# Kernel tuning notes

Hardware: AMD Instinct MI355X
Metric: run time of the kernel (lower is better)

The kernel has to match this reference:

```python
import jax, jax.numpy as jnp
import numpy as np

# Dimensions
N, C_IN, C_OUT, T, V = 64, 64, 64, 256, 25   # batch, channels, frames, joints
K, G = 3, 8                                   # num_subset, groups


def batch_norm(x, gamma, beta, eps=1e-5):
    # BatchNorm2d in training mode: biased batch stats over (N, T, V) per channel.
    mean = jnp.mean(x, axis=(0, 2, 3), keepdims=True)
    var = jnp.var(x, axis=(0, 2, 3), keepdims=True)
    g = gamma.reshape(1, -1, 1, 1)
    b = beta.reshape(1, -1, 1, 1)
    return g * (x - mean) * jax.lax.rsqrt(var + eps) + b


def setup_inputs() -> dict:
    key = jax.random.key(0)
    k0, k1, k2 = jax.random.split(key, 3)
    x0 = jax.random.normal(k0, (N, C_IN, T, V), dtype=jnp.float32)
    # decoupled adjacency parameter [num_subset, groups, V, V] (non-negative, adjacency-like)
    decoupled_A = jax.random.uniform(k1, (K, G, V, V), dtype=jnp.float32)
    scale = float(np.sqrt(0.5 / (C_OUT * K)))
    linear_weight = jax.random.normal(k2, (C_IN, C_OUT * K), dtype=jnp.float32) * scale
    linear_bias = jnp.full((1, C_OUT * K, 1, 1), 1e-6, dtype=jnp.float32)
    bn0_gamma = jnp.ones((C_OUT * K,), dtype=jnp.float32)
    bn0_beta = jnp.zeros((C_OUT * K,), dtype=jnp.float32)
    bn_gamma = jnp.ones((C_OUT,), dtype=jnp.float32)
    bn_beta = jnp.zeros((C_OUT,), dtype=jnp.float32)
    return {
        "x0": x0,
        "decoupled_A": decoupled_A,
        "linear_weight": linear_weight,
        "linear_bias": linear_bias,
        "bn0_gamma": bn0_gamma,
        "bn0_beta": bn0_beta,
        "bn_gamma": bn_gamma,
        "bn_beta": bn_beta,
    }


def reference(x0, decoupled_A, linear_weight, linear_bias,
              bn0_gamma, bn0_beta, bn_gamma, bn_beta):
    # Expand grouped adjacency to per-output-channel: [K, C_OUT, V, V]
    learn_adj = jnp.tile(decoupled_A, (1, C_OUT // G, 1, 1))
    # Degree normalization: A @ diag(1/(colsum+1e-3)) == divide columns by column sums.
    deg = jnp.sum(learn_adj, axis=2, keepdims=True)          # [K, C_OUT, 1, V]
    normed_adj = learn_adj / (deg + 0.001)                    # [K, C_OUT, V, V]

    # Pointwise channel mix: [N, C_IN, T, V] -> [N, K*C_OUT, T, V]
    x = jnp.einsum('nctw,cd->ndtw', x0, linear_weight) + linear_bias
    x = batch_norm(x, bn0_gamma, bn0_beta)

    n, kc, t, v = x.shape
    x = x.reshape(n, K, kc // K, t, v)                        # [N, K, C_OUT, T, V]
    # Per-channel graph propagation summed over subsets.
    x = jnp.einsum('nkctv,kcvw->nctw', x, normed_adj)         # [N, C_OUT, T, V]
    x = batch_norm(x, bn_gamma, bn_beta)

    x = x + x0  # identity residual (in_channels == out_channels)
    return jax.nn.relu(x)
```

## Files before the change

kernel.cpp:

```cpp
#include <hip/hip_runtime.h>
#include <hip/hip_bf16.h>

#define N_    64
#define CIN   64
#define COUT  64
#define T_    256
#define V_    25
#define K_    3
#define G_    8
#define D_    192
#define TV    6400
#define P_    409600.0f

typedef __attribute__((ext_vector_type(8))) short bf16x8;
typedef __attribute__((ext_vector_type(4))) float f32x4;

__device__ __forceinline__ float bf2f(unsigned short u) {
    unsigned int x = ((unsigned int)u) << 16;
    return __uint_as_float(x);
}
__device__ __forceinline__ unsigned short f2bf(float f) {
    unsigned int x = __float_as_uint(f);
    unsigned int lsb = (x >> 16) & 1u;
    x += 0x7fffu + lsb;
    return (unsigned short)(x >> 16);
}

__global__ __launch_bounds__(256, 4) void k1_mfma(const float* __restrict__ x0,
                                                  const float* __restrict__ W,
                                                  const float* __restrict__ bias,
                                                  unsigned short* __restrict__ z) {
    int p0  = blockIdx.x * 256;
    int n   = p0 / TV;
    int tvb = p0 % TV;
    int wv  = threadIdx.x >> 6;
    int l   = threadIdx.x & 63;
    int l15 = l & 15;
    int kg  = l >> 4;
    int wbase = tvb + wv * 64;
    const float* xn = x0 + (size_t)n * CIN * TV;

    bf16x8 afr[4][2];
#pragma unroll
    for (int m = 0; m < 4; ++m)
#pragma unroll
        for (int kk = 0; kk < 2; ++kk)
#pragma unroll
            for (int j = 0; j < 8; ++j) {
                int c = kk * 32 + kg * 8 + j;
                afr[m][kk][j] = (short)f2bf(xn[(size_t)c * TV + wbase + m * 16 + l15]);
            }

    unsigned short* zn = z + (size_t)n * D_ * TV;
#pragma unroll 1
    for (int dt = 0; dt < 12; ++dt) {
        int dcol = dt * 16 + l15;
        bf16x8 bfr[2];
#pragma unroll
        for (int kk = 0; kk < 2; ++kk)
#pragma unroll
            for (int j = 0; j < 8; ++j) {
                int c = kk * 32 + kg * 8 + j;
                bfr[kk][j] = (short)f2bf(W[c * D_ + dcol]);
            }
        float bv = bias[dcol];
        f32x4 acc[4];
#pragma unroll
        for (int m = 0; m < 4; ++m) {
            acc[m][0] = bv; acc[m][1] = bv; acc[m][2] = bv; acc[m][3] = bv;
        }
#pragma unroll
        for (int m = 0; m < 4; ++m) {
            acc[m] = __builtin_amdgcn_mfma_f32_16x16x32_bf16(afr[m][0], bfr[0], acc[m], 0, 0, 0);
            acc[m] = __builtin_amdgcn_mfma_f32_16x16x32_bf16(afr[m][1], bfr[1], acc[m], 0, 0, 0);
        }
        unsigned short* zp = zn + (size_t)dcol * TV;
#pragma unroll
        for (int m = 0; m < 4; ++m) {
            int tv0 = wbase + m * 16 + kg * 4;
            uint2 pk;
            pk.x = (unsigned int)f2bf(acc[m][0]) | ((unsigned int)f2bf(acc[m][1]) << 16);
            pk.y = (unsigned int)f2bf(acc[m][2]) | ((unsigned int)f2bf(acc[m][3]) << 16);
            *(uint2*)(zp + tv0) = pk;
        }
    }
}

__global__ __launch_bounds__(256) void k1b_stats(const unsigned short* __restrict__ z,
                                                 float* __restrict__ sum0,
                                                 float* __restrict__ sumsq0) {
    int d    = blockIdx.x;
    int slab = blockIdx.y;
    float s = 0.f, sq = 0.f;
    for (int n = slab * 8; n < slab * 8 + 8; ++n) {
        const ushort4* zp = (const ushort4*)(z + ((size_t)n * D_ + d) * TV);
        for (int i = threadIdx.x; i < TV / 4; i += 256) {
            ushort4 u = zp[i];
            float a0 = bf2f(u.x), a1 = bf2f(u.y), a2 = bf2f(u.z), a3 = bf2f(u.w);
            s  += (a0 + a1) + (a2 + a3);
            sq += (a0 * a0 + a1 * a1) + (a2 * a2 + a3 * a3);
        }
    }
    __shared__ float rs[256], rq[256];
    rs[threadIdx.x] = s; rq[threadIdx.x] = sq;
    __syncthreads();
    for (int off = 128; off > 0; off >>= 1) {
        if (threadIdx.x < off) {
            rs[threadIdx.x] += rs[threadIdx.x + off];
            rq[threadIdx.x] += rq[threadIdx.x + off];
        }
        __syncthreads();
    }
    if (threadIdx.x == 0) {
        atomicAdd(&sum0[d], rs[0]);
        atomicAdd(&sumsq0[d], rq[0]);
    }
}

__global__ __launch_bounds__(256, 1) void k2_prep(const float* __restrict__ A,
                                                  const float* __restrict__ g0,
                                                  const float* __restrict__ b0,
                                                  const float* __restrict__ sum0,
                                                  const float* __restrict__ sumsq0,
                                                  float* a, float* b,
                                                  float* nadj, float* bconst) {
    int tid = threadIdx.x;
    if (tid < D_) {
        float m   = sum0[tid] / P_;
        float var = sumsq0[tid] / P_ - m * m;
        float sc  = g0[tid] * rsqrtf(var + 1e-5f);
        a[tid] = sc;
        b[tid] = b0[tid] - sc * m;
    }
    for (int idx = tid; idx < K_ * G_ * V_; idx += 256) {
        int w  = idx % V_;
        int kg = idx / V_;
        const float* Ap = A + kg * V_ * V_;
        float cs = 0.f;
        for (int v = 0; v < V_; ++v) cs += Ap[v * V_ + w];
        float inv = 1.f / (cs + 1e-3f);
        for (int v = 0; v < V_; ++v) nadj[kg * V_ * V_ + v * V_ + w] = Ap[v * V_ + w] * inv;
    }
    __syncthreads();
    for (int idx = tid; idx < COUT * V_; idx += 256) {
        int c = idx / V_, w = idx % V_, g = c & 7;
        float s = 0.f;
        for (int k = 0; k < K_; ++k) {
            float bk = b[k * COUT + c];
            const float* np_ = nadj + (k * G_ + g) * V_ * V_;
            float cs = 0.f;
            for (int v = 0; v < V_; ++v) cs += np_[v * V_ + w];
            s += bk * cs;
        }
        bconst[idx] = s;
    }
}

__global__ __launch_bounds__(256, 2) void k3_adj(const unsigned short* __restrict__ z,
                                                 const float* __restrict__ a,
                                                 const float* __restrict__ nadj,
                                                 const float* __restrict__ bconst,
                                                 unsigned short* __restrict__ x2,
                                                 float* __restrict__ sum2,
                                                 float* __restrict__ sumsq2) {
    __shared__ float s_nadj[K_][625];
    __shared__ __align__(16) unsigned short zs[4][TV];
    int tid = threadIdx.x;
    int g   = blockIdx.x & 7;
    int pq  = blockIdx.x >> 3;
    int wv  = tid >> 6;
    int l   = tid & 63;
    int p   = pq * 4 + wv;
    int n   = p >> 3;
    int c   = (p & 7) * 8 + g;
    for (int idx = tid; idx < K_ * 625; idx += 256) {
        int k = idx / 625, r = idx % 625;
        s_nadj[k][r] = nadj[(k * 8 + g) * 625 + r];
    }
    __syncthreads();

    float acc[4][25];
#pragma unroll
    for (int w = 0; w < 25; ++w) {
        float bc = bconst[c * 25 + w];
#pragma unroll
        for (int j = 0; j < 4; ++j) acc[j][w] = bc;
    }

    uint4* zs4 = (uint4*)&zs[wv][0];
#pragma unroll 1
    for (int k = 0; k < K_; ++k) {
        int d = k * 64 + c;
        const uint4* row4 = (const uint4*)(z + ((size_t)n * D_ + d) * TV);
        for (int e = l; e < 800; e += 64) zs4[e] = row4[e];
        float ad = a[d];
#pragma unroll 1
        for (int v = 0; v < 25; ++v) {
            float za0 = ad * bf2f(zs[wv][(l      ) * 25 + v]);
            float za1 = ad * bf2f(zs[wv][(l +  64) * 25 + v]);
            float za2 = ad * bf2f(zs[wv][(l + 128) * 25 + v]);
            float za3 = ad * bf2f(zs[wv][(l + 192) * 25 + v]);
            const float* nr = &s_nadj[k][v * 25];
#pragma unroll
            for (int w = 0; w < 25; ++w) {
                float nv = nr[w];
                acc[0][w] = fmaf(za0, nv, acc[0][w]);
                acc[1][w] = fmaf(za1, nv, acc[1][w]);
                acc[2][w] = fmaf(za2, nv, acc[2][w]);
                acc[3][w] = fmaf(za3, nv, acc[3][w]);
            }
        }
    }

    unsigned short* xp = x2 + ((size_t)n * COUT + c) * TV;
    float s = 0.f, sq = 0.f;
#pragma unroll
    for (int j = 0; j < 4; ++j) {
        int t = l + 64 * j;
#pragma unroll
        for (int w = 0; w < 25; ++w) {
            float val = acc[j][w];
            s += val; sq += val * val;
            xp[t * 25 + w] = f2bf(val);
        }
    }
#pragma unroll
    for (int off = 32; off > 0; off >>= 1) {
        s  += __shfl_down(s,  off, 64);
        sq += __shfl_down(sq, off, 64);
    }
    if (l == 0) {
        atomicAdd(&sum2[c], s);
        atomicAdd(&sumsq2[c], sq);
    }
}

__global__ __launch_bounds__(256) void k4_final(const unsigned short* __restrict__ x2,
                                                const float* __restrict__ x0,
                                                const float* __restrict__ g2,
                                                const float* __restrict__ b2,
                                                const float* __restrict__ sum2,
                                                const float* __restrict__ sumsq2,
                                                float* __restrict__ out) {
    const int total4 = N_ * COUT * TV / 4;
    for (int i = blockIdx.x * 256 + threadIdx.x; i < total4; i += gridDim.x * 256) {
        int c = ((i * 4) / TV) & 63;
        float m   = sum2[c] * (1.f / P_);
        float var = sumsq2[c] * (1.f / P_) - m * m;
        float sc  = g2[c] * rsqrtf(var + 1e-5f);
        float sh  = b2[c] - sc * m;
        ushort4 u = ((const ushort4*)x2)[i];
        float4  x = ((const float4*)x0)[i];
        float4 o;
        o.x = fmaxf(sc * bf2f(u.x) + sh + x.x, 0.f);
        o.y = fmaxf(sc * bf2f(u.y) + sh + x.y, 0.f);
        o.z = fmaxf(sc * bf2f(u.z) + sh + x.z, 0.f);
        o.w = fmaxf(sc * bf2f(u.w) + sh + x.w, 0.f);
        ((float4*)out)[i] = o;
    }
}

extern "C" void kernel_launch(void* const* d_in, const int* in_sizes, int n_in,
                              void* d_out, int out_size, void* d_ws, size_t ws_size,
                              hipStream_t stream) {
    const float* x0   = (const float*)d_in[0];
    const float* A    = (const float*)d_in[1];
    const float* W    = (const float*)d_in[2];
    const float* bias = (const float*)d_in[3];
    const float* g0   = (const float*)d_in[4];
    const float* b0   = (const float*)d_in[5];
    const float* g2   = (const float*)d_in[6];
    const float* b2   = (const float*)d_in[7];

    char* ws = (char*)d_ws;
    unsigned short* z  = (unsigned short*)ws;
    unsigned short* x2 = (unsigned short*)(ws + 157286400ull);
    float* fregion = (float*)(ws + 209715200ull);
    float* sum0   = fregion;
    float* sumsq0 = fregion + 192;
    float* sum2   = fregion + 384;
    float* sumsq2 = fregion + 448;
    float* a      = fregion + 512;
    float* b      = a + 192;
    float* nadj   = b + 192;
    float* bconst = nadj + 15000;

    hipMemsetAsync(fregion, 0, 512 * sizeof(float), stream);
    k1_mfma<<<1600, 256, 0, stream>>>(x0, W, bias, z);
    k1b_stats<<<dim3(D_, 8), 256, 0, stream>>>(z, sum0, sumsq0);
    k2_prep<<<1, 256, 0, stream>>>(A, g0, b0, sum0, sumsq0, a, b, nadj, bconst);
    k3_adj<<<1024, 256, 0, stream>>>(z, a, nadj, bconst, x2, sum2, sumsq2);
    k4_final<<<2048, 256, 0, stream>>>(x2, x0, g2, b2, sum2, sumsq2,
                                       (float*)d_out);
}
```

Baseline: 429.3 us.

## Fuse BN0 statistics into GEMM epilogue and stage z stores through LDS

Per-channel sum and sum-of-squares for the first batch norm are now computed from the fp32 MFMA accumulators inside the GEMM kernel. Per-block partials are written to a scratch buffer, and a small kernel reduces them deterministically. This removes the separate pass that re-read the whole bf16 intermediate z to get the statistics. Output tiles are also transposed through shared memory so the global stores are wider and contiguous. Statistics now come from unrounded fp32 values rather than the bf16-rounded z, which slightly changes numerics.

```diff
diff --git a/kernel.cpp b/kernel.cpp
--- a/kernel.cpp
+++ b/kernel.cpp
@@ -11,6 +11,7 @@
 #define D_    192
 #define TV    6400
 #define P_    409600.0f
+#define NBLK1 1600
 
 typedef __attribute__((ext_vector_type(8))) short bf16x8;
 typedef __attribute__((ext_vector_type(4))) float f32x4;
@@ -29,7 +30,10 @@
 __global__ __launch_bounds__(256, 4) void k1_mfma(const float* __restrict__ x0,
                                                   const float* __restrict__ W,
                                                   const float* __restrict__ bias,
-                                                  unsigned short* __restrict__ z) {
+                                                  unsigned short* __restrict__ z,
+                                                  float* __restrict__ part) {
+    __shared__ unsigned short zb[4][16 * 68];
+    __shared__ float ps[4][12][16], pq[4][12][16];
     int p0  = blockIdx.x * 256;
     int n   = p0 / TV;
     int tvb = p0 % TV;
@@ -52,6 +56,7 @@
             }
 
     unsigned short* zn = z + (size_t)n * D_ * TV;
+    unsigned short* zw = &zb[wv][0];
 #pragma unroll 1
     for (int dt = 0; dt < 12; ++dt) {
         int dcol = dt * 16 + l15;
@@ -74,46 +79,55 @@
             acc[m] = __builtin_amdgcn_mfma_f32_16x16x32_bf16(afr[m][0], bfr[0], acc[m], 0, 0, 0);
             acc[m] = __builtin_amdgcn_mfma_f32_16x16x32_bf16(afr[m][1], bfr[1], acc[m], 0, 0, 0);
         }
-        unsigned short* zp = zn + (size_t)dcol * TV;
+        float s = 0.f, sq = 0.f;
+#pragma unroll
+        for (int m = 0; m < 4; ++m)
+#pragma unroll
+            for (int r = 0; r < 4; ++r) {
+                float v = acc[m][r];
+                s += v; sq += v * v;
+            }
+        s  += __shfl_xor(s, 16, 64);  s  += __shfl_xor(s, 32, 64);
+        sq += __shfl_xor(sq, 16, 64); sq += __shfl_xor(sq, 32, 64);
+        if (kg == 0) { ps[wv][dt][l15] = s; pq[wv][dt][l15] = sq; }
 #pragma unroll
         for (int m = 0; m < 4; ++m) {
-            int tv0 = wbase + m * 16 + kg * 4;
             uint2 pk;
             pk.x = (unsigned int)f2bf(acc[m][0]) | ((unsigned int)f2bf(acc[m][1]) << 16);
             pk.y = (unsigned int)f2bf(acc[m][2]) | ((unsigned int)f2bf(acc[m][3]) << 16);
-            *(uint2*)(zp + tv0) = pk;
-        }
-    }
-}
-
-__global__ __launch_bounds__(256) void k1b_stats(const unsigned short* __restrict__ z,
+            *(uint2*)(&zw[l15 * 68 + m * 16 + kg * 4]) = pk;
+        }
+#pragma unroll
+        for (int i = 0; i < 4; ++i) {
+            int dR  = i * 4 + kg;
+            int tvo = l15 * 4;
+            uint2 v = *(const uint2*)(&zw[dR * 68 + tvo]);
+            *(uint2*)(zn + (size_t)(dt * 16 + dR) * TV + wbase + tvo) = v;
+        }
+    }
+    __syncthreads();
+    int tid = threadIdx.x;
+    if (tid < D_) {
+        int dt = tid >> 4, lo = tid & 15;
+        float s = ps[0][dt][lo] + ps[1][dt][lo] + ps[2][dt][lo] + ps[3][dt][lo];
+        float q = pq[0][dt][lo] + pq[1][dt][lo] + pq[2][dt][lo] + pq[3][dt][lo];
+        part[(size_t)blockIdx.x * 384 + tid]        = s;
+        part[(size_t)blockIdx.x * 384 + 192 + tid]  = q;
+    }
+}
+
+__global__ __launch_bounds__(64) void k1c_reduce(const float* __restrict__ part,
                                                  float* __restrict__ sum0,
                                                  float* __restrict__ sumsq0) {
-    int d    = blockIdx.x;
-    int slab = blockIdx.y;
-    float s = 0.f, sq = 0.f;
-    for (int n = slab * 8; n < slab * 8 + 8; ++n) {
-        const ushort4* zp = (const ushort4*)(z + ((size_t)n * D_ + d) * TV);
-        for (int i = threadIdx.x; i < TV / 4; i += 256) {
-            ushort4 u = zp[i];
-            float a0 = bf2f(u.x), a1 = bf2f(u.y), a2 = bf2f(u.z), a3 = bf2f(u.w);
-            s  += (a0 + a1) + (a2 + a3);
-            sq += (a0 * a0 + a1 * a1) + (a2 * a2 + a3 * a3);
-        }
-    }
-    __shared__ float rs[256], rq[256];
-    rs[threadIdx.x] = s; rq[threadIdx.x] = sq;
-    __syncthreads();
-    for (int off = 128; off > 0; off >>= 1) {
-        if (threadIdx.x < off) {
-            rs[threadIdx.x] += rs[threadIdx.x + off];
-            rq[threadIdx.x] += rq[threadIdx.x + off];
-        }
-        __syncthreads();
-    }
-    if (threadIdx.x == 0) {
-        atomicAdd(&sum0[d], rs[0]);
-        atomicAdd(&sumsq0[d], rq[0]);
+    int idx = blockIdx.x;
+    int l = threadIdx.x;
+    float s = 0.f;
+    for (int b = l; b < NBLK1; b += 64) s += part[(size_t)b * 384 + idx];
+#pragma unroll
+    for (int off = 32; off > 0; off >>= 1) s += __shfl_down(s, off, 64);
+    if (l == 0) {
+        if (idx < D_) sum0[idx] = s;
+        else          sumsq0[idx - D_] = s;
     }
 }
 
@@ -275,6 +289,7 @@
     char* ws = (char*)d_ws;
     unsigned short* z  = (unsigned short*)ws;
     unsigned short* x2 = (unsigned short*)(ws + 157286400ull);
+    float* part = (float*)x2;
     float* fregion = (float*)(ws + 209715200ull);
     float* sum0   = fregion;
     float* sumsq0 = fregion + 192;
@@ -286,8 +301,8 @@
     float* bconst = nadj + 15000;
 
     hipMemsetAsync(fregion, 0, 512 * sizeof(float), stream);
-    k1_mfma<<<1600, 256, 0, stream>>>(x0, W, bias, z);
-    k1b_stats<<<dim3(D_, 8), 256, 0, stream>>>(z, sum0, sumsq0);
+    k1_mfma<<<NBLK1, 256, 0, stream>>>(x0, W, bias, z, part);
+    k1c_reduce<<<384, 64, 0, stream>>>(part, sum0, sumsq0);
     k2_prep<<<1, 256, 0, stream>>>(A, g0, b0, sum0, sumsq0, a, b, nadj, bconst);
     k3_adj<<<1024, 256, 0, stream>>>(z, a, nadj, bconst, x2, sum2, sumsq2);
     k4_final<<<2048, 256, 0, stream>>>(x2, x0, g2, b2, sum2, sumsq2,
```

Result: faster. 395.9 us (-7.8%).
